# Kernel optimization log

Hardware: AMD Instinct MI355X
Metric: run time of the kernel (lower is better)

The kernel has to match this reference:

```python
import jax, jax.numpy as jnp
import numpy as np

N_NODES = 50000   # batch_size * n_verts
N_EDGES = 800000
D_FEAT = 128
UNITS = 256


def setup_inputs() -> dict:
    key = jax.random.key(0)
    k1, k2, k3, k4, k5 = jax.random.split(key, 5)
    features = jax.random.normal(k1, (N_NODES, D_FEAT), dtype=jnp.float32)
    edge_row = jax.random.randint(k2, (N_EDGES,), 0, N_NODES, dtype=jnp.int32)
    edge_col = jax.random.randint(k3, (N_EDGES,), 0, N_NODES, dtype=jnp.int32)
    edge_val = jax.random.uniform(k4, (N_EDGES,), dtype=jnp.float32)
    W = jax.random.normal(k5, (D_FEAT, UNITS), dtype=jnp.float32) * (1.0 / np.sqrt(D_FEAT))
    return {"features": features, "edge_row": edge_row, "edge_col": edge_col,
            "edge_val": edge_val, "W": W}


def reference(features, edge_row, edge_col, edge_val, W):
    # features: [N, F] (already the (batch*n_verts, F) layout the layer reshapes to)
    # A in COO: A[edge_row[e], edge_col[e]] = edge_val[e]
    n = features.shape[0]
    # in_degree = row-sum of A values, +1 for self loop
    in_degree = jax.ops.segment_sum(edge_val, edge_row, num_segments=n) + 1.0
    invsqrt_deg = jax.lax.rsqrt(in_degree)                       # [N]
    normalized = invsqrt_deg[:, None] * features                 # [N, F]
    # pooled = A @ normalized  (gather source rows, scale, scatter-add to dest)
    msgs = edge_val[:, None] * normalized[edge_col]              # [E, F]
    pooled = jax.ops.segment_sum(msgs, edge_row, num_segments=n) # [N, F]
    # self-loop contribution (normalized case)
    pooled = pooled + invsqrt_deg[:, None] * normalized
    # dense projection + relu
    out = jax.nn.relu(pooled @ W)                                # [N, units]
    return out
```

## Files before the change

### kernel.cpp

```cpp
#include <hip/hip_runtime.h>

constexpr int N = 50000;
constexpr int E = 800000;
constexpr int F = 128;
constexpr int U = 256;

typedef __attribute__((ext_vector_type(8))) short short8;
typedef __attribute__((ext_vector_type(4))) float float4v;

__device__ inline unsigned short f32_to_bf16(float x) {
    unsigned int u = __float_as_uint(x);
    unsigned int r = (u + 0x7fffu + ((u >> 16) & 1u)) >> 16;
    return (unsigned short)r;
}

constexpr float FIXED_SCALE = 67108864.0f;
constexpr float FIXED_INV   = 1.4901161193847656e-8f;

__device__ inline float decode_deg(unsigned long long p) {
    return (float)(p & 0xFFFFFFFFFFull) * FIXED_INV;
}

__global__ __launch_bounds__(256) void hist_kernel(const int* __restrict__ erow,
                                                   const float* __restrict__ eval,
                                                   unsigned long long* __restrict__ packed,
                                                   int* __restrict__ rank) {
    int e = blockIdx.x * 256 + threadIdx.x;
    if (e < E) {
        int r = erow[e];
        unsigned long long add =
            (1ull << 40) | (unsigned long long)(eval[e] * FIXED_SCALE);
        unsigned long long old = atomicAdd(&packed[r], add);
        rank[e] = (int)(old >> 40);
    }
}

__global__ __launch_bounds__(256) void blksum_kernel(const unsigned long long* __restrict__ packed,
                                                     int* __restrict__ blk_sum) {
    int i = blockIdx.x * 256 + threadIdx.x;
    int v = (i < N) ? (int)(packed[i] >> 40) : 0;
    #pragma unroll
    for (int off = 32; off > 0; off >>= 1) v += __shfl_down(v, off, 64);
    __shared__ int s[4];
    if ((threadIdx.x & 63) == 0) s[threadIdx.x >> 6] = v;
    __syncthreads();
    if (threadIdx.x == 0) blk_sum[blockIdx.x] = s[0] + s[1] + s[2] + s[3];
}

__global__ __launch_bounds__(256) void scansum_kernel(const int* __restrict__ blk_sum,
                                                      int* __restrict__ blk_off,
                                                      int* __restrict__ row_ptr) {
    __shared__ int sh[256];
    int t = threadIdx.x;
    int v = (t < 196) ? blk_sum[t] : 0;
    sh[t] = v;
    __syncthreads();
    for (int off = 1; off < 256; off <<= 1) {
        int u = (t >= off) ? sh[t - off] : 0;
        __syncthreads();
        sh[t] += u;
        __syncthreads();
    }
    blk_off[t] = sh[t] - v;
    if (t == 0) row_ptr[N] = E;
}

__global__ __launch_bounds__(256) void blkscan_kernel(const unsigned long long* __restrict__ packed,
                                                      const int* __restrict__ blk_off,
                                                      int* __restrict__ row_ptr) {
    __shared__ int sh[256];
    int t = threadIdx.x;
    int i = blockIdx.x * 256 + t;
    int v = (i < N) ? (int)(packed[i] >> 40) : 0;
    sh[t] = v;
    __syncthreads();
    for (int off = 1; off < 256; off <<= 1) {
        int u = (t >= off) ? sh[t - off] : 0;
        __syncthreads();
        sh[t] += u;
        __syncthreads();
    }
    if (i < N) row_ptr[i] = blk_off[blockIdx.x] + sh[t] - v;
}

__global__ __launch_bounds__(256) void permute_kernel(const int* __restrict__ erow,
                                                      const int* __restrict__ ecol,
                                                      const float* __restrict__ eval,
                                                      const int* __restrict__ rank,
                                                      const int* __restrict__ row_ptr,
                                                      int2* __restrict__ csr) {
    int e = blockIdx.x * 256 + threadIdx.x;
    if (e < E) {
        int p = row_ptr[erow[e]] + rank[e];
        csr[p] = make_int2(ecol[e], __float_as_int(eval[e]));
    }
}

__global__ __launch_bounds__(256) void norm_kernel(const float* __restrict__ feat,
                                                   const unsigned long long* __restrict__ packed,
                                                   unsigned short* __restrict__ nrm) {
    int tid = blockIdx.x * 256 + threadIdx.x;
    int node = tid >> 5;
    int q    = tid & 31;
    float iv = rsqrtf(decode_deg(packed[node]) + 1.0f);
    float4 f = ((const float4*)feat)[node * 32 + q];
    ushort4 o;
    o.x = f32_to_bf16(iv * f.x);
    o.y = f32_to_bf16(iv * f.y);
    o.z = f32_to_bf16(iv * f.z);
    o.w = f32_to_bf16(iv * f.w);
    ((ushort4*)nrm)[node * 32 + q] = o;
}

__global__ __launch_bounds__(256) void gather_kernel(const int* __restrict__ row_ptr,
                                                     const int2* __restrict__ csr,
                                                     const unsigned short* __restrict__ nrm,
                                                     const unsigned long long* __restrict__ packed,
                                                     const float* __restrict__ feat,
                                                     unsigned int* __restrict__ pooledb) {
    int gtid = blockIdx.x * 256 + threadIdx.x;
    int n    = gtid >> 6;
    int lane = threadIdx.x & 63;
    if (n >= N) return;

    float iv  = rsqrtf(decode_deg(packed[n]) + 1.0f);
    float iv2 = iv * iv;
    float2 f = ((const float2*)feat)[n * 64 + lane];
    float acc0 = iv2 * f.x;
    float acc1 = iv2 * f.y;

    int e = row_ptr[n], e1 = row_ptr[n + 1];
    for (; e + 3 < e1; e += 4) {
        int2 p0 = csr[e], p1 = csr[e + 1], p2 = csr[e + 2], p3 = csr[e + 3];
        unsigned int u0 = *(const unsigned int*)&nrm[(size_t)p0.x * F + lane * 2];
        unsigned int u1 = *(const unsigned int*)&nrm[(size_t)p1.x * F + lane * 2];
        unsigned int u2 = *(const unsigned int*)&nrm[(size_t)p2.x * F + lane * 2];
        unsigned int u3 = *(const unsigned int*)&nrm[(size_t)p3.x * F + lane * 2];
        float v0 = __int_as_float(p0.y), v1 = __int_as_float(p1.y);
        float v2 = __int_as_float(p2.y), v3 = __int_as_float(p3.y);
        acc0 += v0 * __uint_as_float(u0 << 16);
        acc1 += v0 * __uint_as_float(u0 & 0xffff0000u);
        acc0 += v1 * __uint_as_float(u1 << 16);
        acc1 += v1 * __uint_as_float(u1 & 0xffff0000u);
        acc0 += v2 * __uint_as_float(u2 << 16);
        acc1 += v2 * __uint_as_float(u2 & 0xffff0000u);
        acc0 += v3 * __uint_as_float(u3 << 16);
        acc1 += v3 * __uint_as_float(u3 & 0xffff0000u);
    }
    for (; e < e1; ++e) {
        int2 p0 = csr[e];
        unsigned int u0 = *(const unsigned int*)&nrm[(size_t)p0.x * F + lane * 2];
        float v0 = __int_as_float(p0.y);
        acc0 += v0 * __uint_as_float(u0 << 16);
        acc1 += v0 * __uint_as_float(u0 & 0xffff0000u);
    }
    pooledb[n * 64 + lane] =
        (unsigned int)f32_to_bf16(acc0) | ((unsigned int)f32_to_bf16(acc1) << 16);
}

__global__ __launch_bounds__(256) void wt_kernel(const float* __restrict__ W,
                                                 unsigned short* __restrict__ Wt) {
    int idx = blockIdx.x * 256 + threadIdx.x;
    int k = idx >> 8;
    int n = idx & 255;
    Wt[n * F + k] = f32_to_bf16(W[idx]);
}

__global__ __launch_bounds__(256) void gemm_mfma_kernel(const unsigned short* __restrict__ Ab,
                                                        const unsigned short* __restrict__ Wt,
                                                        float* __restrict__ out) {
    __shared__ unsigned short As[16384];
    __shared__ unsigned short Bs[16384];
    const int tid = threadIdx.x;
    const int m0 = blockIdx.x * 128;
    const int n0 = blockIdx.y * 128;

    {
        const int r = tid >> 1;
        const int h = tid & 1;
        const int grow = m0 + r;
        const uint4* asrc = (grow < N) ? (const uint4*)(Ab + (size_t)grow * F) : nullptr;
        const uint4* bsrc = (const uint4*)(Wt + (size_t)(n0 + r) * F);
        #pragma unroll
        for (int j = 0; j < 8; ++j) {
            int o = h * 8 + j;
            int ks = o >> 2, quad = o & 3;
            int slot = ((ks * 8 + (r >> 4)) * 64) + (quad << 4) + (r & 15);
            uint4 av = asrc ? asrc[o] : make_uint4(0u, 0u, 0u, 0u);
            ((uint4*)As)[slot] = av;
            ((uint4*)Bs)[slot] = bsrc[o];
        }
    }
    __syncthreads();

    const int wave = tid >> 6;
    const int lane = tid & 63;
    float4v acc[8][2];
    #pragma unroll
    for (int i = 0; i < 8; ++i) {
        acc[i][0] = (float4v){0.f, 0.f, 0.f, 0.f};
        acc[i][1] = (float4v){0.f, 0.f, 0.f, 0.f};
    }

    #pragma unroll
    for (int ks = 0; ks < 4; ++ks) {
        short8 b0 = *(const short8*)&Bs[(((ks * 8 + wave * 2 + 0) * 64) + lane) * 8];
        short8 b1 = *(const short8*)&Bs[(((ks * 8 + wave * 2 + 1) * 64) + lane) * 8];
        #pragma unroll
        for (int mt = 0; mt < 8; ++mt) {
            short8 a = *(const short8*)&As[(((ks * 8 + mt) * 64) + lane) * 8];
            acc[mt][0] = __builtin_amdgcn_mfma_f32_16x16x32_bf16(a, b0, acc[mt][0], 0, 0, 0);
            acc[mt][1] = __builtin_amdgcn_mfma_f32_16x16x32_bf16(a, b1, acc[mt][1], 0, 0, 0);
        }
    }

    const int quad = lane >> 4;
    const int colt = lane & 15;
    #pragma unroll
    for (int mt = 0; mt < 8; ++mt) {
        #pragma unroll
        for (int nt = 0; nt < 2; ++nt) {
            int col = n0 + (wave * 2 + nt) * 16 + colt;
            #pragma unroll
            for (int i = 0; i < 4; ++i) {
                int row = m0 + mt * 16 + quad * 4 + i;
                if (row < N) out[(size_t)row * U + col] = fmaxf(acc[mt][nt][i], 0.f);
            }
        }
    }
}

extern "C" void kernel_launch(void* const* d_in, const int* in_sizes, int n_in,
                              void* d_out, int out_size, void* d_ws, size_t ws_size,
                              hipStream_t stream) {
    (void)in_sizes; (void)n_in; (void)out_size; (void)ws_size;

    const float* feat = (const float*)d_in[0];
    const int*   erow = (const int*)d_in[1];
    const int*   ecol = (const int*)d_in[2];
    const float* eval = (const float*)d_in[3];
    const float* W    = (const float*)d_in[4];
    float* out = (float*)d_out;

    char* ws = (char*)d_ws;
    unsigned long long* packed  = (unsigned long long*)(ws + 0);
    int*            row_ptr = (int*)  (ws + 400000);
    int*            blk_sum = (int*)  (ws + 600064);
    int*            blk_off = (int*)  (ws + 601088);
    int*            rank    = (int*)  (ws + 602112);
    int2*           csr     = (int2*) (ws + 3802112);
    unsigned short* Wt      = (unsigned short*)(ws + 10202112);
    unsigned short* nrm     = (unsigned short*)(ws + 10267648);
    unsigned int*   pooledb = (unsigned int*)  (ws + 23067648);

    (void)hipMemsetAsync(ws, 0, 400000, stream);

    hist_kernel<<<(E + 255) / 256, 256, 0, stream>>>(erow, eval, packed, rank);

    const int SBLK = (N + 255) / 256;
    blksum_kernel <<<SBLK, 256, 0, stream>>>(packed, blk_sum);
    scansum_kernel<<<1,    256, 0, stream>>>(blk_sum, blk_off, row_ptr);
    blkscan_kernel<<<SBLK, 256, 0, stream>>>(packed, blk_off, row_ptr);

    permute_kernel<<<(E + 255) / 256, 256, 0, stream>>>(erow, ecol, eval, rank, row_ptr, csr);
    norm_kernel<<<(N * 32) / 256, 256, 0, stream>>>(feat, packed, nrm);
    wt_kernel<<<(F * U) / 256, 256, 0, stream>>>(W, Wt);
    gather_kernel<<<(N * 64) / 256, 256, 0, stream>>>(row_ptr, csr, nrm, packed, feat, pooledb);

    dim3 ggrid((N + 127) / 128, U / 128);
    gemm_mfma_kernel<<<ggrid, 256, 0, stream>>>((const unsigned short*)pooledb, Wt, out);
}
```

Baseline: 219.0 us.

## Split histogram counters into 8 sub-buckets per row to cut atomic contention

The row histogram now keys each edge by row*8 plus a block-derived slot, so atomics spread over 8 counters per row and use 32-bit ints instead of packed 64-bit fixed-point adds. Degree sums are no longer accumulated atomically; norm_kernel instead reduces edge values from the CSR per node and stores the inverse square root for the gather. The W transpose is folded into the histogram launch. The trade-off is an 8x larger counter array, a larger prefix scan, and an extra pass over CSR values.

Measured after the change: 219.7 us. About the same (+0.3%).

```diff
diff --git a/kernel.cpp b/kernel.cpp
--- a/kernel.cpp
+++ b/kernel.cpp
@@ -5,6 +5,12 @@
 constexpr int F = 128;
 constexpr int U = 256;
 
+constexpr int R    = 8;
+constexpr int NK   = N * R;
+constexpr int EBLK = E / 256;
+constexpr int SBLK = (NK + 255) / 256;
+constexpr int CH   = (SBLK + 255) / 256;
+
 typedef __attribute__((ext_vector_type(8))) short short8;
 typedef __attribute__((ext_vector_type(4))) float float4v;
 
@@ -14,31 +20,27 @@
     return (unsigned short)r;
 }
 
-constexpr float FIXED_SCALE = 67108864.0f;
-constexpr float FIXED_INV   = 1.4901161193847656e-8f;
-
-__device__ inline float decode_deg(unsigned long long p) {
-    return (float)(p & 0xFFFFFFFFFFull) * FIXED_INV;
-}
-
 __global__ __launch_bounds__(256) void hist_kernel(const int* __restrict__ erow,
-                                                   const float* __restrict__ eval,
-                                                   unsigned long long* __restrict__ packed,
-                                                   int* __restrict__ rank) {
+                                                   int* __restrict__ cnt,
+                                                   int* __restrict__ rank,
+                                                   const float* __restrict__ W,
+                                                   unsigned short* __restrict__ Wt) {
+    if (blockIdx.x >= EBLK) {
+        int idx = (blockIdx.x - EBLK) * 256 + threadIdx.x;
+        int k = idx >> 8;
+        int n = idx & 255;
+        Wt[n * F + k] = f32_to_bf16(W[idx]);
+        return;
+    }
     int e = blockIdx.x * 256 + threadIdx.x;
-    if (e < E) {
-        int r = erow[e];
-        unsigned long long add =
-            (1ull << 40) | (unsigned long long)(eval[e] * FIXED_SCALE);
-        unsigned long long old = atomicAdd(&packed[r], add);
-        rank[e] = (int)(old >> 40);
-    }
-}
-
-__global__ __launch_bounds__(256) void blksum_kernel(const unsigned long long* __restrict__ packed,
+    int key = erow[e] * R + (blockIdx.x & (R - 1));
+    rank[e] = atomicAdd(&cnt[key], 1);
+}
+
+__global__ __launch_bounds__(256) void blksum_kernel(const int* __restrict__ cnt,
                                                      int* __restrict__ blk_sum) {
     int i = blockIdx.x * 256 + threadIdx.x;
-    int v = (i < N) ? (int)(packed[i] >> 40) : 0;
+    int v = (i < NK) ? cnt[i] : 0;
     #pragma unroll
     for (int off = 32; off > 0; off >>= 1) v += __shfl_down(v, off, 64);
     __shared__ int s[4];
@@ -49,11 +51,19 @@
 
 __global__ __launch_bounds__(256) void scansum_kernel(const int* __restrict__ blk_sum,
                                                       int* __restrict__ blk_off,
-                                                      int* __restrict__ row_ptr) {
+                                                      int* __restrict__ rp2) {
     __shared__ int sh[256];
     int t = threadIdx.x;
-    int v = (t < 196) ? blk_sum[t] : 0;
-    sh[t] = v;
+    int loc[CH];
+    int s = 0;
+    #pragma unroll
+    for (int i = 0; i < CH; ++i) {
+        int idx = t * CH + i;
+        int v = (idx < SBLK) ? blk_sum[idx] : 0;
+        loc[i] = v;
+        s += v;
+    }
+    sh[t] = s;
     __syncthreads();
     for (int off = 1; off < 256; off <<= 1) {
         int u = (t >= off) ? sh[t - off] : 0;
@@ -61,17 +71,25 @@
         sh[t] += u;
         __syncthreads();
     }
-    blk_off[t] = sh[t] - v;
-    if (t == 0) row_ptr[N] = E;
-}
-
-__global__ __launch_bounds__(256) void blkscan_kernel(const unsigned long long* __restrict__ packed,
+    int run = sh[t] - s;
+    #pragma unroll
+    for (int i = 0; i < CH; ++i) {
+        int idx = t * CH + i;
+        if (idx < SBLK) {
+            blk_off[idx] = run;
+            run += loc[i];
+        }
+    }
+    if (t == 0) rp2[NK] = E;
+}
+
+__global__ __launch_bounds__(256) void blkscan_kernel(const int* __restrict__ cnt,
                                                       const int* __restrict__ blk_off,
-                                                      int* __restrict__ row_ptr) {
+                                                      int* __restrict__ rp2) {
     __shared__ int sh[256];
     int t = threadIdx.x;
     int i = blockIdx.x * 256 + t;
-    int v = (i < N) ? (int)(packed[i] >> 40) : 0;
+    int v = (i < NK) ? cnt[i] : 0;
     sh[t] = v;
     __syncthreads();
     for (int off = 1; off < 256; off <<= 1) {
@@ -80,42 +98,50 @@
         sh[t] += u;
         __syncthreads();
     }
-    if (i < N) row_ptr[i] = blk_off[blockIdx.x] + sh[t] - v;
+    if (i < NK) rp2[i] = blk_off[blockIdx.x] + sh[t] - v;
 }
 
 __global__ __launch_bounds__(256) void permute_kernel(const int* __restrict__ erow,
                                                       const int* __restrict__ ecol,
                                                       const float* __restrict__ eval,
                                                       const int* __restrict__ rank,
-                                                      const int* __restrict__ row_ptr,
+                                                      const int* __restrict__ rp2,
                                                       int2* __restrict__ csr) {
     int e = blockIdx.x * 256 + threadIdx.x;
     if (e < E) {
-        int p = row_ptr[erow[e]] + rank[e];
+        int key = erow[e] * R + (blockIdx.x & (R - 1));
+        int p = rp2[key] + rank[e];
         csr[p] = make_int2(ecol[e], __float_as_int(eval[e]));
     }
 }
 
 __global__ __launch_bounds__(256) void norm_kernel(const float* __restrict__ feat,
-                                                   const unsigned long long* __restrict__ packed,
-                                                   unsigned short* __restrict__ nrm) {
-    int tid = blockIdx.x * 256 + threadIdx.x;
-    int node = tid >> 5;
-    int q    = tid & 31;
-    float iv = rsqrtf(decode_deg(packed[node]) + 1.0f);
-    float4 f = ((const float4*)feat)[node * 32 + q];
-    ushort4 o;
-    o.x = f32_to_bf16(iv * f.x);
-    o.y = f32_to_bf16(iv * f.y);
-    o.z = f32_to_bf16(iv * f.z);
-    o.w = f32_to_bf16(iv * f.w);
-    ((ushort4*)nrm)[node * 32 + q] = o;
-}
-
-__global__ __launch_bounds__(256) void gather_kernel(const int* __restrict__ row_ptr,
+                                                   const int* __restrict__ rp2,
+                                                   const int2* __restrict__ csr,
+                                                   float* __restrict__ iv,
+                                                   unsigned int* __restrict__ nrm) {
+    int gtid = blockIdx.x * 256 + threadIdx.x;
+    int n    = gtid >> 6;
+    int lane = threadIdx.x & 63;
+    if (n >= N) return;
+
+    int e0 = rp2[n * R], e1 = rp2[n * R + R];
+    float s = 0.f;
+    for (int e = e0 + lane; e < e1; e += 64) s += __int_as_float(csr[e].y);
+    #pragma unroll
+    for (int off = 32; off > 0; off >>= 1) s += __shfl_xor(s, off, 64);
+    float iv_ = rsqrtf(s + 1.0f);
+    if (lane == 0) iv[n] = iv_;
+
+    float2 f = ((const float2*)feat)[n * 64 + lane];
+    nrm[n * 64 + lane] =
+        (unsigned int)f32_to_bf16(iv_ * f.x) | ((unsigned int)f32_to_bf16(iv_ * f.y) << 16);
+}
+
+__global__ __launch_bounds__(256) void gather_kernel(const int* __restrict__ rp2,
                                                      const int2* __restrict__ csr,
                                                      const unsigned short* __restrict__ nrm,
-                                                     const unsigned long long* __restrict__ packed,
+                                                     const float* __restrict__ iv,
                                                      const float* __restrict__ feat,
                                                      unsigned int* __restrict__ pooledb) {
     int gtid = blockIdx.x * 256 + threadIdx.x;
@@ -123,13 +149,13 @@
     int lane = threadIdx.x & 63;
     if (n >= N) return;
 
-    float iv  = rsqrtf(decode_deg(packed[n]) + 1.0f);
-    float iv2 = iv * iv;
+    float iv_ = iv[n];
+    float iv2 = iv_ * iv_;
     float2 f = ((const float2*)feat)[n * 64 + lane];
     float acc0 = iv2 * f.x;
     float acc1 = iv2 * f.y;
 
-    int e = row_ptr[n], e1 = row_ptr[n + 1];
+    int e = rp2[n * R], e1 = rp2[n * R + R];
     for (; e + 3 < e1; e += 4) {
         int2 p0 = csr[e], p1 = csr[e + 1], p2 = csr[e + 2], p3 = csr[e + 3];
         unsigned int u0 = *(const unsigned int*)&nrm[(size_t)p0.x * F + lane * 2];
@@ -158,14 +184,6 @@
         (unsigned int)f32_to_bf16(acc0) | ((unsigned int)f32_to_bf16(acc1) << 16);
 }
 
-__global__ __launch_bounds__(256) void wt_kernel(const float* __restrict__ W,
-                                                 unsigned short* __restrict__ Wt) {
-    int idx = blockIdx.x * 256 + threadIdx.x;
-    int k = idx >> 8;
-    int n = idx & 255;
-    Wt[n * F + k] = f32_to_bf16(W[idx]);
-}
-
 __global__ __launch_bounds__(256) void gemm_mfma_kernel(const unsigned short* __restrict__ Ab,
                                                         const unsigned short* __restrict__ Wt,
                                                         float* __restrict__ out) {
@@ -243,29 +261,28 @@
     float* out = (float*)d_out;
 
     char* ws = (char*)d_ws;
-    unsigned long long* packed  = (unsigned long long*)(ws + 0);
-    int*            row_ptr = (int*)  (ws + 400000);
-    int*            blk_sum = (int*)  (ws + 600064);
-    int*            blk_off = (int*)  (ws + 601088);
-    int*            rank    = (int*)  (ws + 602112);
-    int2*           csr     = (int2*) (ws + 3802112);
-    unsigned short* Wt      = (unsigned short*)(ws + 10202112);
-    unsigned short* nrm     = (unsigned short*)(ws + 10267648);
-    unsigned int*   pooledb = (unsigned int*)  (ws + 23067648);
-
-    (void)hipMemsetAsync(ws, 0, 400000, stream);
-
-    hist_kernel<<<(E + 255) / 256, 256, 0, stream>>>(erow, eval, packed, rank);
-
-    const int SBLK = (N + 255) / 256;
-    blksum_kernel <<<SBLK, 256, 0, stream>>>(packed, blk_sum);
-    scansum_kernel<<<1,    256, 0, stream>>>(blk_sum, blk_off, row_ptr);
-    blkscan_kernel<<<SBLK, 256, 0, stream>>>(packed, blk_off, row_ptr);
-
-    permute_kernel<<<(E + 255) / 256, 256, 0, stream>>>(erow, ecol, eval, rank, row_ptr, csr);
-    norm_kernel<<<(N * 32) / 256, 256, 0, stream>>>(feat, packed, nrm);
-    wt_kernel<<<(F * U) / 256, 256, 0, stream>>>(W, Wt);
-    gather_kernel<<<(N * 64) / 256, 256, 0, stream>>>(row_ptr, csr, nrm, packed, feat, pooledb);
+    int*            cnt     = (int*)  (ws + 0);
+    int*            rp2     = (int*)  (ws + 1600000);
+    int*            blk_sum = (int*)  (ws + 3200064);
+    int*            blk_off = (int*)  (ws + 3206336);
+    int*            rank    = (int*)  (ws + 3212608);
+    int2*           csr     = (int2*) (ws + 6412608);
+    float*          iv      = (float*)(ws + 12812608);
+    unsigned short* Wt      = (unsigned short*)(ws + 13012608);
+    unsigned short* nrm     = (unsigned short*)(ws + 13078144);
+    unsigned int*   pooledb = (unsigned int*)  (ws + 25878144);
+
+    (void)hipMemsetAsync(cnt, 0, (size_t)NK * sizeof(int), stream);
+
+    hist_kernel<<<EBLK + (F * U) / 256, 256, 0, stream>>>(erow, cnt, rank, W, Wt);
+
+    blksum_kernel <<<SBLK, 256, 0, stream>>>(cnt, blk_sum);
+    scansum_kernel<<<1,    256, 0, stream>>>(blk_sum, blk_off, rp2);
+    blkscan_kernel<<<SBLK, 256, 0, stream>>>(cnt, blk_off, rp2);
+
+    permute_kernel<<<EBLK, 256, 0, stream>>>(erow, ecol, eval, rank, rp2, csr);
+    norm_kernel  <<<(N * 64) / 256, 256, 0, stream>>>(feat, rp2, csr, iv, (unsigned int*)nrm);
+    gather_kernel<<<(N * 64) / 256, 256, 0, stream>>>(rp2, csr, nrm, iv, feat, pooledb);
 
     dim3 ggrid((N + 127) / 128, U / 128);
     gemm_mfma_kernel<<<ggrid, 256, 0, stream>>>((const unsigned short*)pooledb, Wt, out);
```
